# Performance work log

Measured on AMD Instinct MI355X. Metric: run time of the kernel, lower is better.

## Reference

```python
import jax, jax.numpy as jnp
import numpy as np

B, T, D, U = 128, 512, 128, 512


def setup_inputs() -> dict:
    key = jax.random.key(0)
    kx, kwx, kwh = jax.random.split(key, 3)
    x = jax.random.normal(kx, (B, T, D), dtype=jnp.float32)
    Wx = jax.random.normal(kwx, (D, U), dtype=jnp.float32) * (1.0 / np.sqrt(D))
    Wh = jax.random.normal(kwh, (U, U), dtype=jnp.float32) * (1.0 / np.sqrt(U))
    b = jnp.zeros((U,), dtype=jnp.float32)
    return {"x": x, "Wx": Wx, "Wh": Wh, "b": b}


def reference(x, Wx, Wh, b):
    # Elman RNN: h_t = tanh(x_t @ Wx + h_{t-1} @ Wh + b)
    # Faithful to MyRNN(return_sequences=True): TensorArray.stack() -> [T, B, U]
    h0 = jnp.zeros((x.shape[0], Wh.shape[0]), dtype=x.dtype)  # fallback zero initial state
    xs = jnp.swapaxes(x, 0, 1)  # [T, B, D] for scan over time

    def step(h, x_t):
        h_new = jnp.tanh(x_t @ Wx + h @ Wh + b)
        return h_new, h_new

    _, seq = jax.lax.scan(step, h0, xs)
    return seq  # [T, B, U]
```

## Files before the change

kernel.cpp:

```cpp
#include <hip/hip_runtime.h>
#include <stddef.h>
#include <stdint.h>


constexpr int B = 128;
constexpr int T = 512;
constexpr int D = 128;
constexpr int U = 512;

typedef _Float16 f16;
typedef _Float16 f16x2 __attribute__((ext_vector_type(2)));
typedef __fp16   fp16x2 __attribute__((ext_vector_type(2)));
typedef unsigned int u32;
typedef u32 u32x16 __attribute__((ext_vector_type(16)));

union U32H2 { u32 u; f16x2 h; fp16x2 p; };

static __device__ __forceinline__ u32 pk(float a, float b) {
    U32H2 c; c.p = __builtin_amdgcn_cvt_pkrtz(a, b); return c.u;
}

#if __has_builtin(__builtin_amdgcn_fdot2)
static __device__ __forceinline__ float fdot2(u32 a, u32 b, float c) {
    U32H2 x, y; x.u = a; y.u = b;
    return __builtin_amdgcn_fdot2(x.h, y.h, c, false);
}
#else
static __device__ __forceinline__ float fdot2(u32 a, u32 b, float c) {
    U32H2 x, y; x.u = a; y.u = b;
    return c + (float)x.h.x * (float)y.h.x + (float)x.h.y * (float)y.h.y;
}
#endif

static __device__ __forceinline__ float fast_tanh(float x) {
    float e = __expf(2.0f * x);
    return 1.0f - 2.0f * __builtin_amdgcn_rcpf(e + 1.0f);
}

__global__ __launch_bounds__(256) void pgemm_kernel(
    const float* __restrict__ x,
    const float* __restrict__ Wx,
    const float* __restrict__ bias,
    float* __restrict__ P)
{
    __shared__ u32 xs[128][66];
    __shared__ u32 ws[64][132];

    const int rb  = blockIdx.x;
    const int cb  = blockIdx.y;
    const int tid = threadIdx.x;
    const int tr  = tid >> 4;
    const int tcc = tid & 15;

    const float4* x4 = (const float4*)x;
#pragma unroll
    for (int l = 0; l < 16; ++l) {
        int idx = tid + l * 256;
        int r   = idx >> 5;
        int q   = idx & 31;
        int m   = rb * 128 + r;
        int b_  = m & 127;
        int t_  = m >> 7;
        float4 v = x4[((size_t)b_ * T + t_) * 32 + q];
        xs[r][2 * q]     = pk(v.x, v.y);
        xs[r][2 * q + 1] = pk(v.z, v.w);
    }
    const float4* W4 = (const float4*)Wx;
#pragma unroll
    for (int l = 0; l < 8; ++l) {
        int idx = tid + l * 256;
        int kp  = idx >> 5;
        int q   = idx & 31;
        float4 a = W4[(size_t)(2 * kp)     * 128 + cb * 32 + q];
        float4 c = W4[(size_t)(2 * kp + 1) * 128 + cb * 32 + q];
        uint4 w;
        w.x = pk(a.x, c.x); w.y = pk(a.y, c.y);
        w.z = pk(a.z, c.z); w.w = pk(a.w, c.w);
        *(uint4*)&ws[kp][4 * q] = w;
    }
    __syncthreads();

    float acc[8][8];
#pragma unroll
    for (int i = 0; i < 8; ++i)
#pragma unroll
        for (int j = 0; j < 8; ++j) acc[i][j] = 0.f;

#pragma unroll 2
    for (int kp = 0; kp < 64; ++kp) {
        u32 xv[8], wv[8];
#pragma unroll
        for (int i = 0; i < 8; ++i) xv[i] = xs[tr + 16 * i][kp];
#pragma unroll
        for (int j = 0; j < 8; ++j) wv[j] = ws[kp][tcc + 16 * j];
#pragma unroll
        for (int i = 0; i < 8; ++i)
#pragma unroll
            for (int j = 0; j < 8; ++j)
                acc[i][j] = fdot2(xv[i], wv[j], acc[i][j]);
    }

#pragma unroll
    for (int j = 0; j < 8; ++j) {
        int c    = cb * 128 + tcc + 16 * j;
        float bv = bias[c];
#pragma unroll
        for (int i = 0; i < 8; ++i) {
            int m = rb * 128 + tr + 16 * i;
            P[(size_t)m * U + c] = acc[i][j] + bv;
        }
    }
}

__global__ __launch_bounds__(512)
__attribute__((amdgpu_waves_per_eu(2, 2)))
void rnn_kernel(
    const float* __restrict__ Wh,
    float* __restrict__ out)
{
    __shared__ __align__(16) u32 WhL[32768];
    __shared__ __align__(16) u32 part[16 * 264];
    __shared__ __align__(16) u32 hbuf[320];

    const int tid = threadIdx.x;
    const int tk  = tid >> 5;
    const int tc  = tid & 31;
    const int b   = blockIdx.x;

    u32x16 W0, W1, W2, W3, W4, W5, W6, W7, W8, W9, W10, W11;
#define LOADW(q)                                                          \
    {                                                                     \
        const float* r0 = Wh + (size_t)((tk * 16 + (q)) * 2) * U + tc;    \
        _Pragma("unroll")                                                 \
        for (int j = 0; j < 16; ++j)                                      \
            W##q[j] = pk(r0[32 * j], r0[U + 32 * j]);                     \
    }
    LOADW(0)  LOADW(1)  LOADW(2)  LOADW(3)
    LOADW(4)  LOADW(5)  LOADW(6)  LOADW(7)
    LOADW(8)  LOADW(9)  LOADW(10) LOADW(11)
#undef LOADW

#pragma unroll
    for (int pl2 = 0; pl2 < 4; ++pl2) {
        const float* r0 = Wh + (size_t)((tk * 16 + 12 + pl2) * 2) * U + tc;
#pragma unroll
        for (int jc = 0; jc < 4; ++jc) {
            uint4 w;
            w.x = pk(r0[32 * (4 * jc + 0)], r0[U + 32 * (4 * jc + 0)]);
            w.y = pk(r0[32 * (4 * jc + 1)], r0[U + 32 * (4 * jc + 1)]);
            w.z = pk(r0[32 * (4 * jc + 2)], r0[U + 32 * (4 * jc + 2)]);
            w.w = pk(r0[32 * (4 * jc + 3)], r0[U + 32 * (4 * jc + 3)]);
            *(uint4*)&WhL[((pl2 * 4 + jc) * 512 + tid) * 4] = w;
        }
    }

    if (tid < 320) hbuf[tid] = 0u;
    __syncthreads();

    float* outb = out + (size_t)b * U;
    f16* hb16 = (f16*)hbuf;
    const int p0    = tid >> 1;
    const int hidx  = 2 * (p0 + 4 * (p0 >> 4)) + (tid & 1);

    const uint4* WL4 = (const uint4*)WhL;

    float pv0 = 0.f, pv1 = 0.f;
    if (tid < 256) { pv0 = outb[tid]; pv1 = outb[tid + 256]; }

    for (int t = 0; t < T; ++t) {
        int tn = (t + 1 < T) ? (t + 1) : t;
        const float* prown = outb + (size_t)tn * (B * U);
        float nv0 = 0.f, nv1 = 0.f;
        if (tid < 256) { nv0 = prown[tid]; nv1 = prown[tid + 256]; }

        const uint4* h4p = (const uint4*)&hbuf[20 * tk];
        uint4 hv0 = h4p[0];
        uint4 hv1 = h4p[1];
        uint4 hv2 = h4p[2];
        uint4 hv3 = h4p[3];

        uint4 wa = WL4[0 * 512 + tid];
        uint4 wb = WL4[1 * 512 + tid];
        uint4 wc = WL4[2 * 512 + tid];
        uint4 wd = WL4[3 * 512 + tid];

        float acc[16];
#pragma unroll
        for (int j = 0; j < 16; ++j) acc[j] = 0.f;

#define DOT16(hq, Wq)                                                     \
        {                                                                 \
            u32 hq_ = (hq);                                               \
            _Pragma("unroll")                                             \
            for (int j = 0; j < 16; ++j)                                  \
                acc[j] = fdot2(hq_, Wq[j], acc[j]);                       \
        }
        DOT16(hv0.x, W0) DOT16(hv0.y, W1) DOT16(hv0.z, W2) DOT16(hv0.w, W3)
        DOT16(hv1.x, W4) DOT16(hv1.y, W5) DOT16(hv1.z, W6) DOT16(hv1.w, W7)

        uint4 we = WL4[4 * 512 + tid];
        uint4 wf = WL4[5 * 512 + tid];
        uint4 wg = WL4[6 * 512 + tid];
        uint4 wh = WL4[7 * 512 + tid];

        DOT16(hv2.x, W8) DOT16(hv2.y, W9) DOT16(hv2.z, W10) DOT16(hv2.w, W11)
#undef DOT16

#define CONSUME(hq, Aq, Bq, Cq, Dq)                                       \
        {                                                                 \
            u32 hq_ = (hq);                                               \
            acc[0]  = fdot2(hq_, Aq.x, acc[0]);                           \
            acc[1]  = fdot2(hq_, Aq.y, acc[1]);                           \
            acc[2]  = fdot2(hq_, Aq.z, acc[2]);                           \
            acc[3]  = fdot2(hq_, Aq.w, acc[3]);                           \
            acc[4]  = fdot2(hq_, Bq.x, acc[4]);                           \
            acc[5]  = fdot2(hq_, Bq.y, acc[5]);                           \
            acc[6]  = fdot2(hq_, Bq.z, acc[6]);                           \
            acc[7]  = fdot2(hq_, Bq.w, acc[7]);                           \
            acc[8]  = fdot2(hq_, Cq.x, acc[8]);                           \
            acc[9]  = fdot2(hq_, Cq.y, acc[9]);                           \
            acc[10] = fdot2(hq_, Cq.z, acc[10]);                          \
            acc[11] = fdot2(hq_, Cq.w, acc[11]);                          \
            acc[12] = fdot2(hq_, Dq.x, acc[12]);                          \
            acc[13] = fdot2(hq_, Dq.y, acc[13]);                          \
            acc[14] = fdot2(hq_, Dq.z, acc[14]);                          \
            acc[15] = fdot2(hq_, Dq.w, acc[15]);                          \
        }
        CONSUME(hv3.x, wa, wb, wc, wd)
        wa = WL4[ 8 * 512 + tid];
        wb = WL4[ 9 * 512 + tid];
        wc = WL4[10 * 512 + tid];
        wd = WL4[11 * 512 + tid];
        CONSUME(hv3.y, we, wf, wg, wh)
        we = WL4[12 * 512 + tid];
        wf = WL4[13 * 512 + tid];
        wg = WL4[14 * 512 + tid];
        wh = WL4[15 * 512 + tid];
        CONSUME(hv3.z, wa, wb, wc, wd)
        CONSUME(hv3.w, we, wf, wg, wh)
#undef CONSUME

#pragma unroll
        for (int j = 0; j < 8; ++j)
            part[tk * 264 + tc + 32 * j] = pk(acc[j], acc[j + 8]);

        __syncthreads();

        if (tid < 256) {
            float s0 = pv0, s1 = pv1;
#pragma unroll
            for (int i = 0; i < 16; ++i) {
                U32H2 w; w.u = part[i * 264 + tid];
                s0 += (float)w.h.x;
                s1 += (float)w.h.y;
            }
            float h0 = fast_tanh(s0);
            float h1 = fast_tanh(s1);
            float* prow = outb + (size_t)t * (B * U);
            prow[tid]        = h0;
            prow[tid + 256]  = h1;
            hb16[hidx]       = (f16)h0;
            hb16[hidx + 320] = (f16)h1;
        }
        pv0 = nv0; pv1 = nv1;

        __syncthreads();
    }
}

extern "C" void kernel_launch(void* const* d_in, const int* in_sizes, int n_in,
                              void* d_out, int out_size, void* d_ws, size_t ws_size,
                              hipStream_t stream)
{
    (void)d_ws; (void)ws_size; (void)in_sizes; (void)n_in; (void)out_size;
    const float* x    = (const float*)d_in[0];
    const float* Wx   = (const float*)d_in[1];
    const float* Wh   = (const float*)d_in[2];
    const float* bias = (const float*)d_in[3];
    float* out = (float*)d_out;

    pgemm_kernel<<<dim3((T * B) / 128, U / 128), 256, 0, stream>>>(x, Wx, bias, out);
    rnn_kernel<<<B, 512, 0, stream>>>(Wh, out);
}
```

Before: 989.9 us.

## Prefetch LDS weights across steps and halve LDS reduction via wave shuffles

Moves the first eight LDS weight-vector loads for each timestep to the end of the previous iteration, so they overlap the reduction and tanh phase. It interleaves the register-resident dot products with the LDS-weight dot products. Partial sums are combined across the two half-waves with a shuffle before being written, so only 8 partial rows go to shared memory instead of 16. The hidden state is packed by neighbour shuffles into a double-buffered, unpadded buffer, and the final sum uses a tree. This adds live registers for the prefetched weights and extra shuffles, and still keeps two barriers per step.

```diff
diff --git a/kernel.cpp b/kernel.cpp
--- a/kernel.cpp
+++ b/kernel.cpp
@@ -119,12 +119,13 @@
     float* __restrict__ out)
 {
     __shared__ __align__(16) u32 WhL[32768];
-    __shared__ __align__(16) u32 part[16 * 264];
-    __shared__ __align__(16) u32 hbuf[320];
+    __shared__ __align__(16) u32 part[2][2112];
+    __shared__ __align__(16) u32 hbuf[2][256];
 
     const int tid = threadIdx.x;
     const int tk  = tid >> 5;
     const int tc  = tid & 31;
+    const int wv  = tid >> 6;
     const int b   = blockIdx.x;
 
     u32x16 W0, W1, W2, W3, W4, W5, W6, W7, W8, W9, W10, W11;
@@ -154,35 +155,33 @@
         }
     }
 
-    if (tid < 320) hbuf[tid] = 0u;
+    if (tid < 256) hbuf[0][tid] = 0u;
     __syncthreads();
 
+    const uint4* WL4 = (const uint4*)WhL;
     float* outb = out + (size_t)b * U;
-    f16* hb16 = (f16*)hbuf;
-    const int p0    = tid >> 1;
-    const int hidx  = 2 * (p0 + 4 * (p0 >> 4)) + (tid & 1);
-
-    const uint4* WL4 = (const uint4*)WhL;
+
+    uint4 wa = WL4[0 * 512 + tid], wb = WL4[1 * 512 + tid];
+    uint4 wc = WL4[2 * 512 + tid], wd = WL4[3 * 512 + tid];
+    uint4 we = WL4[4 * 512 + tid], wf = WL4[5 * 512 + tid];
+    uint4 wg = WL4[6 * 512 + tid], wh = WL4[7 * 512 + tid];
 
     float pv0 = 0.f, pv1 = 0.f;
     if (tid < 256) { pv0 = outb[tid]; pv1 = outb[tid + 256]; }
 
     for (int t = 0; t < T; ++t) {
+        const int par = t & 1;
+
         int tn = (t + 1 < T) ? (t + 1) : t;
         const float* prown = outb + (size_t)tn * (B * U);
         float nv0 = 0.f, nv1 = 0.f;
         if (tid < 256) { nv0 = prown[tid]; nv1 = prown[tid + 256]; }
 
-        const uint4* h4p = (const uint4*)&hbuf[20 * tk];
-        uint4 hv0 = h4p[0];
-        uint4 hv1 = h4p[1];
-        uint4 hv2 = h4p[2];
-        uint4 hv3 = h4p[3];
-
-        uint4 wa = WL4[0 * 512 + tid];
-        uint4 wb = WL4[1 * 512 + tid];
-        uint4 wc = WL4[2 * 512 + tid];
-        uint4 wd = WL4[3 * 512 + tid];
+        const uint4* hb4 = (const uint4*)hbuf[par];
+        uint4 hv0 = hb4[4 * tk + 0];
+        uint4 hv1 = hb4[4 * tk + 1];
+        uint4 hv2 = hb4[4 * tk + 2];
+        uint4 hv3 = hb4[4 * tk + 3];
 
         float acc[16];
 #pragma unroll
@@ -195,17 +194,6 @@
             for (int j = 0; j < 16; ++j)                                  \
                 acc[j] = fdot2(hq_, Wq[j], acc[j]);                       \
         }
-        DOT16(hv0.x, W0) DOT16(hv0.y, W1) DOT16(hv0.z, W2) DOT16(hv0.w, W3)
-        DOT16(hv1.x, W4) DOT16(hv1.y, W5) DOT16(hv1.z, W6) DOT16(hv1.w, W7)
-
-        uint4 we = WL4[4 * 512 + tid];
-        uint4 wf = WL4[5 * 512 + tid];
-        uint4 wg = WL4[6 * 512 + tid];
-        uint4 wh = WL4[7 * 512 + tid];
-
-        DOT16(hv2.x, W8) DOT16(hv2.y, W9) DOT16(hv2.z, W10) DOT16(hv2.w, W11)
-#undef DOT16
-
 #define CONSUME(hq, Aq, Bq, Cq, Dq)                                       \
         {                                                                 \
             u32 hq_ = (hq);                                               \
@@ -226,45 +214,67 @@
             acc[14] = fdot2(hq_, Dq.z, acc[14]);                          \
             acc[15] = fdot2(hq_, Dq.w, acc[15]);                          \
         }
+        DOT16(hv0.x, W0) DOT16(hv0.y, W1) DOT16(hv0.z, W2) DOT16(hv0.w, W3)
+        DOT16(hv1.x, W4) DOT16(hv1.y, W5) DOT16(hv1.z, W6) DOT16(hv1.w, W7)
+
         CONSUME(hv3.x, wa, wb, wc, wd)
-        wa = WL4[ 8 * 512 + tid];
-        wb = WL4[ 9 * 512 + tid];
-        wc = WL4[10 * 512 + tid];
-        wd = WL4[11 * 512 + tid];
+        wa = WL4[ 8 * 512 + tid]; wb = WL4[ 9 * 512 + tid];
+        wc = WL4[10 * 512 + tid]; wd = WL4[11 * 512 + tid];
+
+        DOT16(hv2.x, W8) DOT16(hv2.y, W9) DOT16(hv2.z, W10) DOT16(hv2.w, W11)
+
         CONSUME(hv3.y, we, wf, wg, wh)
-        we = WL4[12 * 512 + tid];
-        wf = WL4[13 * 512 + tid];
-        wg = WL4[14 * 512 + tid];
-        wh = WL4[15 * 512 + tid];
+        we = WL4[12 * 512 + tid]; wf = WL4[13 * 512 + tid];
+        wg = WL4[14 * 512 + tid]; wh = WL4[15 * 512 + tid];
+
         CONSUME(hv3.z, wa, wb, wc, wd)
+        wa = WL4[0 * 512 + tid]; wb = WL4[1 * 512 + tid];
+        wc = WL4[2 * 512 + tid]; wd = WL4[3 * 512 + tid];
+
         CONSUME(hv3.w, we, wf, wg, wh)
+        we = WL4[4 * 512 + tid]; wf = WL4[5 * 512 + tid];
+        wg = WL4[6 * 512 + tid]; wh = WL4[7 * 512 + tid];
 #undef CONSUME
-
-#pragma unroll
-        for (int j = 0; j < 8; ++j)
-            part[tk * 264 + tc + 32 * j] = pk(acc[j], acc[j + 8]);
+#undef DOT16
+
+#pragma unroll
+        for (int j = 0; j < 16; ++j) acc[j] += __shfl_xor(acc[j], 32);
+
+        if (!(tid & 32)) {
+#pragma unroll
+            for (int j = 0; j < 8; ++j)
+                part[par][wv * 264 + tc + 32 * j] = pk(acc[j], acc[j + 8]);
+        }
 
         __syncthreads();
 
         if (tid < 256) {
-            float s0 = pv0, s1 = pv1;
-#pragma unroll
-            for (int i = 0; i < 16; ++i) {
-                U32H2 w; w.u = part[i * 264 + tid];
-                s0 += (float)w.h.x;
-                s1 += (float)w.h.y;
+            float a0[8], a1[8];
+#pragma unroll
+            for (int i = 0; i < 8; ++i) {
+                U32H2 w; w.u = part[par][i * 264 + tid];
+                a0[i] = (float)w.h.x;
+                a1[i] = (float)w.h.y;
             }
+            float s0 = pv0 + (((a0[0] + a0[1]) + (a0[2] + a0[3]))
+                            + ((a0[4] + a0[5]) + (a0[6] + a0[7])));
+            float s1 = pv1 + (((a1[0] + a1[1]) + (a1[2] + a1[3]))
+                            + ((a1[4] + a1[5]) + (a1[6] + a1[7])));
             float h0 = fast_tanh(s0);
             float h1 = fast_tanh(s1);
             float* prow = outb + (size_t)t * (B * U);
-            prow[tid]        = h0;
-            prow[tid + 256]  = h1;
-            hb16[hidx]       = (f16)h0;
-            hb16[hidx + 320] = (f16)h1;
-        }
+            prow[tid]       = h0;
+            prow[tid + 256] = h1;
+            float o0 = __shfl_xor(h0, 1);
+            float o1 = __shfl_xor(h1, 1);
+            if (!(tid & 1)) {
+                hbuf[par ^ 1][tid >> 1]         = pk(h0, o0);
+                hbuf[par ^ 1][128 + (tid >> 1)] = pk(h1, o1);
+            }
+        }
+
+        __syncthreads();
         pv0 = nv0; pv1 = nv1;
-
-        __syncthreads();
     }
 }
 
```

After: 1.650 ms. 1.67x slower.
